# Kernel tuning notes

Hardware: AMD Instinct MI355X
Metric: run time of the kernel (lower is better)

Reference implementation:

```python
import jax, jax.numpy as jnp
import numpy as np

B, T, D, H = 2, 2048, 512, 8
HD = D // H  # head_dim = 64


def setup_inputs() -> dict:
    key = jax.random.key(0)
    k1, k2, k3, k4 = jax.random.split(key, 4)
    scale = 1.0 / np.sqrt(D)
    x = jax.random.normal(k1, (B, T, D), dtype=jnp.float32)
    periods = jax.random.randint(k2, (B, H), 0, 64, dtype=jnp.int32)
    w_qkv = jax.random.normal(k3, (3 * D, D), dtype=jnp.float32) * scale
    b_qkv = jnp.zeros((3 * D,), dtype=jnp.float32)
    w_out = jax.random.normal(k4, (D, D), dtype=jnp.float32) * scale
    b_out = jnp.zeros((D,), dtype=jnp.float32)
    return {"x": x, "periods": periods, "w_qkv": w_qkv, "b_qkv": b_qkv,
            "w_out": w_out, "b_out": b_out}


def reference(x, periods, w_qkv, b_qkv, w_out, b_out):
    # qkv projection: (B,T,3D) -> (3,B,H,T,HD)
    qkv = x @ w_qkv.T + b_qkv
    qkv = qkv.reshape(B, T, 3, H, HD).transpose(2, 0, 3, 1, 4)
    q, k, v = qkv[0], qkv[1], qkv[2]

    # periodic-causal mask: valid iff j <= i and (i-j) % p == 0, p = max(period,1)
    i_idx = jnp.arange(T, dtype=jnp.int32)[:, None]   # (T,1)
    j_idx = jnp.arange(T, dtype=jnp.int32)[None, :]   # (1,T)
    diff = i_idx - j_idx                              # (T,T)
    p = jnp.maximum(periods, 1)[:, :, None, None]     # (B,H,1,1)
    valid = (diff >= 0) & ((diff % p) == 0)           # (B,H,T,T)

    scores = jnp.einsum('bhqd,bhkd->bhqk', q, k) / np.sqrt(HD)
    scores = jnp.where(valid, scores, jnp.finfo(scores.dtype).min)
    attn = jax.nn.softmax(scores, axis=-1)

    out = jnp.einsum('bhqk,bhkd->bhqd', attn, v)
    out = out.transpose(0, 2, 1, 3).reshape(B, T, D)
    return out @ w_out.T + b_out
```

## Files before the change

### kernel.cpp

```cpp
#include <hip/hip_runtime.h>
#include <math.h>

#define B_  2
#define T_  2048
#define D_  512
#define H_  8
#define HD_ 64
#define QKVS (3*D_)

typedef __bf16 bf16x8 __attribute__((ext_vector_type(8)));
typedef float  f32x4  __attribute__((ext_vector_type(4)));

__device__ inline unsigned short f2bf(float f) {
  unsigned int u = __float_as_uint(f);
  return (unsigned short)((u + 0x7FFFu + ((u >> 16) & 1u)) >> 16);
}
__device__ inline unsigned int pack2bf(float lo, float hi) {
  return (unsigned int)f2bf(lo) | ((unsigned int)f2bf(hi) << 16);
}

__global__ void cast_all(const float* __restrict__ x,
                         const float* __restrict__ wq,
                         const float* __restrict__ wo,
                         unsigned short* __restrict__ xb,
                         unsigned short* __restrict__ wqb,
                         unsigned short* __restrict__ wob) {
  const int n_x  = (B_ * T_ * D_) / 4;
  const int n_wq = (QKVS * D_) / 4;
  const int n_wo = (D_ * D_) / 4;
  int i = blockIdx.x * blockDim.x + threadIdx.x;
  const float* src; unsigned short* dst; int off;
  if (i < n_x)                { src = x;  dst = xb;  off = i; }
  else if (i < n_x + n_wq)    { src = wq; dst = wqb; off = i - n_x; }
  else if (i < n_x + n_wq + n_wo) { src = wo; dst = wob; off = i - n_x - n_wq; }
  else return;
  float4 v = ((const float4*)src)[off];
  ushort4 o;
  o.x = f2bf(v.x); o.y = f2bf(v.y); o.z = f2bf(v.z); o.w = f2bf(v.w);
  ((ushort4*)dst)[off] = o;
}

template<int BF16OUT>
__global__ __launch_bounds__(256)
void gemm_nt_mfma(const unsigned short* __restrict__ A,
                  const unsigned short* __restrict__ Bw,
                  const float* __restrict__ bias, void* __restrict__ Cv,
                  int M, int N, int K) {
  __shared__ short Asd[128 * 32];
  __shared__ short Bsd[64 * 32];

  const int tid = threadIdx.x;
  const int w   = tid >> 6;
  const int l   = tid & 63;
  const int wr  = w >> 1;
  const int wc  = w & 1;
  const int q   = l >> 4;
  const int ml  = l & 15;
  const int arow = l >> 2;
  const int kch  = (l & 3) * 8;

  const int rowbase = blockIdx.y * 128;
  const int colbase = blockIdx.x * 64;

  f32x4 acc[4][2] = {};

  for (int k0 = 0; k0 < K; k0 += 32) {
    __syncthreads();
    #pragma unroll
    for (int s = 0; s < 2; ++s) {
      const unsigned short* g =
          A + (size_t)(rowbase + s * 64 + w * 16 + arow) * K + k0 + kch;
      short* lp = &Asd[s * 2048 + w * 512];
      __builtin_amdgcn_global_load_lds(
          (const __attribute__((address_space(1))) void*)g,
          (__attribute__((address_space(3))) void*)lp, 16, 0, 0);
    }
    {
      const unsigned short* g =
          Bw + (size_t)(colbase + w * 16 + arow) * K + k0 + kch;
      short* lp = &Bsd[w * 512];
      __builtin_amdgcn_global_load_lds(
          (const __attribute__((address_space(1))) void*)g,
          (__attribute__((address_space(3))) void*)lp, 16, 0, 0);
    }
    __syncthreads();

    bf16x8 af[4], bfr[2];
    #pragma unroll
    for (int mi = 0; mi < 4; ++mi)
      af[mi] = *(const bf16x8*)&Asd[(wr * 64 + mi * 16 + ml) * 32 + q * 8];
    #pragma unroll
    for (int ni = 0; ni < 2; ++ni)
      bfr[ni] = *(const bf16x8*)&Bsd[(wc * 32 + ni * 16 + ml) * 32 + q * 8];
    #pragma unroll
    for (int mi = 0; mi < 4; ++mi)
      #pragma unroll
      for (int ni = 0; ni < 2; ++ni)
        acc[mi][ni] = __builtin_amdgcn_mfma_f32_16x16x32_bf16(
            af[mi], bfr[ni], acc[mi][ni], 0, 0, 0);
  }

  #pragma unroll
  for (int mi = 0; mi < 4; ++mi) {
    #pragma unroll
    for (int ni = 0; ni < 2; ++ni) {
      const int col = colbase + wc * 32 + ni * 16 + ml;
      const float bv = bias[col];
      #pragma unroll
      for (int r = 0; r < 4; ++r) {
        const int row = rowbase + wr * 64 + mi * 16 + q * 4 + r;
        const float val = acc[mi][ni][r] + bv;
        if (BF16OUT)
          ((unsigned short*)Cv)[(size_t)row * N + col] = f2bf(val);
        else
          ((float*)Cv)[(size_t)row * N + col] = val;
      }
    }
  }
}

template<int BF16OUT>
__global__ __launch_bounds__(256)
void gemm_nt_mfma128(const unsigned short* __restrict__ A,
                     const unsigned short* __restrict__ Bw,
                     const float* __restrict__ bias, void* __restrict__ Cv,
                     int M, int N, int K) {
  __shared__ short Asd[128 * 32];
  __shared__ short Bsd[128 * 32];

  const int tid = threadIdx.x;
  const int w   = tid >> 6;
  const int l   = tid & 63;
  const int wr  = w >> 1;
  const int wc  = w & 1;
  const int q   = l >> 4;
  const int ml  = l & 15;
  const int arow = l >> 2;
  const int kch  = (l & 3) * 8;

  const int rowbase = blockIdx.y * 128;
  const int colbase = blockIdx.x * 128;

  f32x4 acc[4][4] = {};

  for (int k0 = 0; k0 < K; k0 += 32) {
    __syncthreads();
    #pragma unroll
    for (int s = 0; s < 2; ++s) {
      const unsigned short* ga =
          A + (size_t)(rowbase + s * 64 + w * 16 + arow) * K + k0 + kch;
      __builtin_amdgcn_global_load_lds(
          (const __attribute__((address_space(1))) void*)ga,
          (__attribute__((address_space(3))) void*)&Asd[s * 2048 + w * 512],
          16, 0, 0);
      const unsigned short* gb =
          Bw + (size_t)(colbase + s * 64 + w * 16 + arow) * K + k0 + kch;
      __builtin_amdgcn_global_load_lds(
          (const __attribute__((address_space(1))) void*)gb,
          (__attribute__((address_space(3))) void*)&Bsd[s * 2048 + w * 512],
          16, 0, 0);
    }
    __syncthreads();

    bf16x8 af[4], bfr[4];
    #pragma unroll
    for (int mi = 0; mi < 4; ++mi)
      af[mi] = *(const bf16x8*)&Asd[(wr * 64 + mi * 16 + ml) * 32 + q * 8];
    #pragma unroll
    for (int ni = 0; ni < 4; ++ni)
      bfr[ni] = *(const bf16x8*)&Bsd[(wc * 64 + ni * 16 + ml) * 32 + q * 8];
    #pragma unroll
    for (int mi = 0; mi < 4; ++mi)
      #pragma unroll
      for (int ni = 0; ni < 4; ++ni)
        acc[mi][ni] = __builtin_amdgcn_mfma_f32_16x16x32_bf16(
            af[mi], bfr[ni], acc[mi][ni], 0, 0, 0);
  }

  #pragma unroll
  for (int mi = 0; mi < 4; ++mi) {
    #pragma unroll
    for (int ni = 0; ni < 4; ++ni) {
      const int col = colbase + wc * 64 + ni * 16 + ml;
      const float bv = bias[col];
      #pragma unroll
      for (int r = 0; r < 4; ++r) {
        const int row = rowbase + wr * 64 + mi * 16 + q * 4 + r;
        const float val = acc[mi][ni][r] + bv;
        if (BF16OUT)
          ((unsigned short*)Cv)[(size_t)row * N + col] = f2bf(val);
        else
          ((float*)Cv)[(size_t)row * N + col] = val;
      }
    }
  }
}

__global__ __launch_bounds__(256)
void attn_flash2(const unsigned short* __restrict__ qkv,
                 const int* __restrict__ periods,
                 unsigned short* __restrict__ ao) {
  const int bh = blockIdx.x, slot = blockIdx.y;
  int p = periods[bh]; if (p < 1) p = 1;
  const int g  = slot / p;
  const int r  = slot - g * p;
  const int L  = (T_ - 1 - r) / p + 1;
  const int q0 = g << 6;
  if (q0 >= L) return;
  const int b = bh >> 3, h = bh & 7;
  const int Lrem = L - q0;
  const int Nkb  = min(L, q0 + 64);

  const int tid  = threadIdx.x;
  const int w    = tid >> 6;
  const int lane = tid & 63;
  const int Q = lane >> 4, c = lane & 15;

  __shared__ __align__(16) unsigned short Qs[64 * 72];
  __shared__ __align__(16) unsigned short Ks[32 * 72];
  __shared__ __align__(16) unsigned short Vt[64 * 40];

  const size_t rowb = (size_t)b * T_ * QKVS + (size_t)h * HD_;

  {
    const int u = tid >> 2, ch4 = (tid & 3) * 16;
    const int t = q0 + min(u, Lrem - 1);
    const unsigned short* gq = qkv + rowb + (size_t)(r + t * p) * QKVS + ch4;
    int4 v0 = ((const int4*)gq)[0];
    int4 v1 = ((const int4*)gq)[1];
    *(int4*)&Qs[u * 72 + ch4 + 0] = v0;
    *(int4*)&Qs[u * 72 + ch4 + 8] = v1;
  }
  __syncthreads();
  bf16x8 qf[2];
  qf[0] = *(const bf16x8*)&Qs[(w * 16 + c) * 72 + Q * 8];
  qf[1] = *(const bf16x8*)&Qs[(w * 16 + c) * 72 + Q * 8 + 32];

  const int qb      = w * 16;
  const int nqw     = min(16, Lrem - qb);
  const int qglob   = q0 + qb + c;
  const int mylastk = q0 + qb + 15;

  float m_run = -3.0e38f, l_run = 0.f;
  f32x4 o[4] = {};
  const size_t kb = rowb + D_;
  const size_t vb = rowb + 2 * D_;

  const int krow = tid >> 3, koff = (tid & 7) * 8;
  const int vkey = tid & 31, vd0 = (tid >> 5) * 8;

  for (int k0 = 0; k0 < Nkb; k0 += 32) {
    {
      const int tk = min(k0 + krow, Nkb - 1);
      const int tv = min(k0 + vkey, Nkb - 1);
      int4 kv = *(const int4*)(qkv + kb + (size_t)(r + tk * p) * QKVS + koff);
      int4 vv = *(const int4*)(qkv + vb + (size_t)(r + tv * p) * QKVS + vd0);
      unsigned short vh[8];
      *(int4*)vh = vv;
      __syncthreads();
      *(int4*)&Ks[krow * 72 + koff] = kv;
      #pragma unroll
      for (int j = 0; j < 8; ++j)
        Vt[(vd0 + j) * 40 + vkey] = vh[j];
      __syncthreads();
    }

    if (nqw > 0 && k0 <= mylastk) {
      f32x4 s[2];
      #pragma unroll
      for (int mt = 0; mt < 2; ++mt) {
        bf16x8 a0 = *(const bf16x8*)&Ks[(mt * 16 + c) * 72 + Q * 8];
        bf16x8 a1 = *(const bf16x8*)&Ks[(mt * 16 + c) * 72 + Q * 8 + 32];
        f32x4 acc = {};
        acc = __builtin_amdgcn_mfma_f32_16x16x32_bf16(a0, qf[0], acc, 0, 0, 0);
        acc = __builtin_amdgcn_mfma_f32_16x16x32_bf16(a1, qf[1], acc, 0, 0, 0);
        s[mt] = acc;
      }

      float pvv[8];
      float tmax = -3.0e38f;
      #pragma unroll
      for (int mt = 0; mt < 2; ++mt)
        #pragma unroll
        for (int rg = 0; rg < 4; ++rg) {
          const int kk = k0 + mt * 16 + Q * 4 + rg;
          float v = s[mt][rg] * 0.125f;
          v = (kk <= qglob) ? v : -3.0e38f;
          pvv[mt * 4 + rg] = v;
          tmax = fmaxf(tmax, v);
        }
      tmax = fmaxf(tmax, __shfl_xor(tmax, 16));
      tmax = fmaxf(tmax, __shfl_xor(tmax, 32));
      const float m_new = fmaxf(m_run, tmax);
      const float alpha = __expf(m_run - m_new);
      float tsum = 0.f;
      #pragma unroll
      for (int i = 0; i < 8; ++i) { pvv[i] = __expf(pvv[i] - m_new); tsum += pvv[i]; }
      tsum += __shfl_xor(tsum, 16);
      tsum += __shfl_xor(tsum, 32);
      l_run = l_run * alpha + tsum;
      m_run = m_new;

      unsigned int pk0[2], pk1[2];
      pk0[0] = pack2bf(pvv[0], pvv[1]); pk0[1] = pack2bf(pvv[2], pvv[3]);
      pk1[0] = pack2bf(pvv[4], pvv[5]); pk1[1] = pack2bf(pvv[6], pvv[7]);
      int dw[4];
      const int sq2 = (Q & 1) << 1;
      #pragma unroll
      for (int d = 0; d < 4; ++d) {
        const int src = ((sq2 + (d >> 1)) << 4) + c;
        const int v0 = __shfl((int)pk0[d & 1], src);
        const int v1 = __shfl((int)pk1[d & 1], src);
        dw[d] = (Q >= 2) ? v1 : v0;
      }
      int4 bi = make_int4(dw[0], dw[1], dw[2], dw[3]);
      bf16x8 pb = *(bf16x8*)&bi;

      #pragma unroll
      for (int ch = 0; ch < 4; ++ch) {
        bf16x8 af = *(const bf16x8*)&Vt[(ch * 16 + c) * 40 + Q * 8];
        f32x4 oo = o[ch];
        #pragma unroll
        for (int t2 = 0; t2 < 4; ++t2) oo[t2] *= alpha;
        o[ch] = __builtin_amdgcn_mfma_f32_16x16x32_bf16(af, pb, oo, 0, 0, 0);
      }
    }
  }

  if (nqw > 0 && c < nqw) {
    const float invl = 1.f / l_run;
    const int tok = r + (q0 + qb + c) * p;
    unsigned int* dst =
        (unsigned int*)(ao + (size_t)(b * T_ + tok) * D_ + h * HD_);
    #pragma unroll
    for (int ch = 0; ch < 4; ++ch)
      #pragma unroll
      for (int rp = 0; rp < 2; ++rp) {
        const int dhalf = ch * 16 + Q * 4 + rp * 2;
        dst[dhalf >> 1] =
            pack2bf(o[ch][rp * 2] * invl, o[ch][rp * 2 + 1] * invl);
      }
  }
}

extern "C" void kernel_launch(void* const* d_in, const int* in_sizes, int n_in,
                              void* d_out, int out_size, void* d_ws, size_t ws_size,
                              hipStream_t stream) {
  const float* x      = (const float*)d_in[0];
  const int*   period = (const int*)  d_in[1];
  const float* w_qkv  = (const float*)d_in[2];
  const float* b_qkv  = (const float*)d_in[3];
  const float* w_out  = (const float*)d_in[4];
  const float* b_out  = (const float*)d_in[5];
  float* out = (float*)d_out;

  const int M = B_ * T_;

  char* ws = (char*)d_ws;
  unsigned short* xb   = (unsigned short*)(ws);
  unsigned short* wqb  = (unsigned short*)(ws + (size_t)M * D_ * 2);
  unsigned short* wob  = (unsigned short*)(ws + (size_t)M * D_ * 2
                                              + (size_t)QKVS * D_ * 2);
  unsigned short* qkvb = (unsigned short*)(ws + (size_t)M * D_ * 2
                                              + (size_t)QKVS * D_ * 2
                                              + (size_t)D_ * D_ * 2);
  unsigned short* aob  = xb;

  {
    const int n4 = (M * D_ + QKVS * D_ + D_ * D_) / 4;
    cast_all<<<dim3((n4 + 255) / 256), dim3(256), 0, stream>>>(
        x, w_qkv, w_out, xb, wqb, wob);
  }

  gemm_nt_mfma128<1><<<dim3(QKVS / 128, M / 128), dim3(256), 0, stream>>>(
      xb, wqb, b_qkv, qkvb, M, QKVS, D_);

  attn_flash2<<<dim3(16, 63), dim3(256), 0, stream>>>(qkvb, period, aob);

  gemm_nt_mfma<0><<<dim3(D_ / 64, M / 128), dim3(256), 0, stream>>>(
      aob, wob, b_out, out, M, D_, D_);
}
```

Before: 116.6 us.

## Scatter QKV into period-grouped contiguous planes and use single-wave attention tiles

```diff
diff --git a/kernel.cpp b/kernel.cpp
--- a/kernel.cpp
+++ b/kernel.cpp
@@ -30,8 +30,8 @@
   const int n_wo = (D_ * D_) / 4;
   int i = blockIdx.x * blockDim.x + threadIdx.x;
   const float* src; unsigned short* dst; int off;
-  if (i < n_x)                { src = x;  dst = xb;  off = i; }
-  else if (i < n_x + n_wq)    { src = wq; dst = wqb; off = i - n_x; }
+  if (i < n_x)                    { src = x;  dst = xb;  off = i; }
+  else if (i < n_x + n_wq)        { src = wq; dst = wqb; off = i - n_x; }
   else if (i < n_x + n_wq + n_wo) { src = wo; dst = wob; off = i - n_x - n_wq; }
   else return;
   float4 v = ((const float4*)src)[off];
@@ -40,91 +40,15 @@
   ((ushort4*)dst)[off] = o;
 }
 
-template<int BF16OUT>
 __global__ __launch_bounds__(256)
-void gemm_nt_mfma(const unsigned short* __restrict__ A,
-                  const unsigned short* __restrict__ Bw,
-                  const float* __restrict__ bias, void* __restrict__ Cv,
-                  int M, int N, int K) {
-  __shared__ short Asd[128 * 32];
-  __shared__ short Bsd[64 * 32];
-
-  const int tid = threadIdx.x;
-  const int w   = tid >> 6;
-  const int l   = tid & 63;
-  const int wr  = w >> 1;
-  const int wc  = w & 1;
-  const int q   = l >> 4;
-  const int ml  = l & 15;
-  const int arow = l >> 2;
-  const int kch  = (l & 3) * 8;
-
-  const int rowbase = blockIdx.y * 128;
-  const int colbase = blockIdx.x * 64;
-
-  f32x4 acc[4][2] = {};
-
-  for (int k0 = 0; k0 < K; k0 += 32) {
-    __syncthreads();
-    #pragma unroll
-    for (int s = 0; s < 2; ++s) {
-      const unsigned short* g =
-          A + (size_t)(rowbase + s * 64 + w * 16 + arow) * K + k0 + kch;
-      short* lp = &Asd[s * 2048 + w * 512];
-      __builtin_amdgcn_global_load_lds(
-          (const __attribute__((address_space(1))) void*)g,
-          (__attribute__((address_space(3))) void*)lp, 16, 0, 0);
-    }
-    {
-      const unsigned short* g =
-          Bw + (size_t)(colbase + w * 16 + arow) * K + k0 + kch;
-      short* lp = &Bsd[w * 512];
-      __builtin_amdgcn_global_load_lds(
-          (const __attribute__((address_space(1))) void*)g,
-          (__attribute__((address_space(3))) void*)lp, 16, 0, 0);
-    }
-    __syncthreads();
-
-    bf16x8 af[4], bfr[2];
-    #pragma unroll
-    for (int mi = 0; mi < 4; ++mi)
-      af[mi] = *(const bf16x8*)&Asd[(wr * 64 + mi * 16 + ml) * 32 + q * 8];
-    #pragma unroll
-    for (int ni = 0; ni < 2; ++ni)
-      bfr[ni] = *(const bf16x8*)&Bsd[(wc * 32 + ni * 16 + ml) * 32 + q * 8];
-    #pragma unroll
-    for (int mi = 0; mi < 4; ++mi)
-      #pragma unroll
-      for (int ni = 0; ni < 2; ++ni)
-        acc[mi][ni] = __builtin_amdgcn_mfma_f32_16x16x32_bf16(
-            af[mi], bfr[ni], acc[mi][ni], 0, 0, 0);
-  }
-
-  #pragma unroll
-  for (int mi = 0; mi < 4; ++mi) {
-    #pragma unroll
-    for (int ni = 0; ni < 2; ++ni) {
-      const int col = colbase + wc * 32 + ni * 16 + ml;
-      const float bv = bias[col];
-      #pragma unroll
-      for (int r = 0; r < 4; ++r) {
-        const int row = rowbase + wr * 64 + mi * 16 + q * 4 + r;
-        const float val = acc[mi][ni][r] + bv;
-        if (BF16OUT)
-          ((unsigned short*)Cv)[(size_t)row * N + col] = f2bf(val);
-        else
-          ((float*)Cv)[(size_t)row * N + col] = val;
-      }
-    }
-  }
-}
-
-template<int BF16OUT>
-__global__ __launch_bounds__(256)
-void gemm_nt_mfma128(const unsigned short* __restrict__ A,
-                     const unsigned short* __restrict__ Bw,
-                     const float* __restrict__ bias, void* __restrict__ Cv,
-                     int M, int N, int K) {
+void gemm_qkv(const unsigned short* __restrict__ A,
+              const unsigned short* __restrict__ Bw,
+              const float* __restrict__ bias,
+              const int* __restrict__ periods,
+              unsigned short* __restrict__ Qr,
+              unsigned short* __restrict__ Kr,
+              unsigned short* __restrict__ Vr,
+              int M, int N, int K) {
   __shared__ short Asd[128 * 32];
   __shared__ short Bsd[128 * 32];
 
@@ -177,135 +101,161 @@
             af[mi], bfr[ni], acc[mi][ni], 0, 0, 0);
   }
 
+  const int colb = colbase + wc * 64;
+  const int sec  = colb >> 9;
+  const int h    = (colb >> 6) & 7;
+  const int bidx = rowbase >> 11;
+  unsigned short* plane =
+      (sec == 0 ? Qr : (sec == 1 ? Kr : Vr)) +
+      (size_t)(bidx * 8 + h) * (T_ * HD_);
+  unsigned int pp = (unsigned int)periods[bidx * 8 + h];
+  if ((int)pp < 1) pp = 1;
+  const unsigned int qd = 2048u / pp;
+  const unsigned int md = 2048u - qd * pp;
+
   #pragma unroll
   for (int mi = 0; mi < 4; ++mi) {
     #pragma unroll
-    for (int ni = 0; ni < 4; ++ni) {
-      const int col = colbase + wc * 64 + ni * 16 + ml;
-      const float bv = bias[col];
-      #pragma unroll
-      for (int r = 0; r < 4; ++r) {
-        const int row = rowbase + wr * 64 + mi * 16 + q * 4 + r;
-        const float val = acc[mi][ni][r] + bv;
-        if (BF16OUT)
-          ((unsigned short*)Cv)[(size_t)row * N + col] = f2bf(val);
-        else
-          ((float*)Cv)[(size_t)row * N + col] = val;
+    for (int r2 = 0; r2 < 4; ++r2) {
+      const unsigned int t =
+          (unsigned int)((rowbase + wr * 64 + mi * 16 + q * 4 + r2) & 2047);
+      const unsigned int ti = t / pp;
+      const unsigned int rr = t - ti * pp;
+      const unsigned int pos = rr * qd + (rr < md ? rr : md) + ti;
+      #pragma unroll
+      for (int ni = 0; ni < 4; ++ni) {
+        const int col = colb + ni * 16 + ml;
+        plane[(size_t)pos * HD_ + ni * 16 + ml] =
+            f2bf(acc[mi][ni][r2] + bias[col]);
       }
     }
   }
 }
 
 __global__ __launch_bounds__(256)
-void attn_flash2(const unsigned short* __restrict__ qkv,
+void transpose_v(const unsigned short* __restrict__ Vr,
+                 unsigned short* __restrict__ VTr) {
+  const int bh = blockIdx.x, chunk = blockIdx.y;
+  const int pos0 = chunk * 128;
+  __shared__ unsigned short Ls[128 * 72];
+  const int tid = threadIdx.x;
+  {
+    const int row = tid >> 1, off = (tid & 1) * 32;
+    const unsigned short* src = Vr + ((size_t)bh * T_ + pos0 + row) * HD_ + off;
+    int4 v0 = ((const int4*)src)[0];
+    int4 v1 = ((const int4*)src)[1];
+    int4 v2 = ((const int4*)src)[2];
+    int4 v3 = ((const int4*)src)[3];
+    *(int4*)&Ls[row * 72 + off + 0]  = v0;
+    *(int4*)&Ls[row * 72 + off + 8]  = v1;
+    *(int4*)&Ls[row * 72 + off + 16] = v2;
+    *(int4*)&Ls[row * 72 + off + 24] = v3;
+  }
+  __syncthreads();
+  {
+    const int d = tid >> 2, po = (tid & 3) * 32;
+    unsigned int wv[16];
+    #pragma unroll
+    for (int i = 0; i < 16; ++i) {
+      unsigned short lo = Ls[(po + 2 * i) * 72 + d];
+      unsigned short hi = Ls[(po + 2 * i + 1) * 72 + d];
+      wv[i] = (unsigned int)lo | ((unsigned int)hi << 16);
+    }
+    unsigned short* dst = VTr + ((size_t)bh * HD_ + d) * T_ + pos0 + po;
+    ((int4*)dst)[0] = make_int4(wv[0],  wv[1],  wv[2],  wv[3]);
+    ((int4*)dst)[1] = make_int4(wv[4],  wv[5],  wv[6],  wv[7]);
+    ((int4*)dst)[2] = make_int4(wv[8],  wv[9],  wv[10], wv[11]);
+    ((int4*)dst)[3] = make_int4(wv[12], wv[13], wv[14], wv[15]);
+  }
+}
+
+__global__ __launch_bounds__(64)
+void attn_flash3(const unsigned short* __restrict__ Qr,
+                 const unsigned short* __restrict__ Kr,
+                 const unsigned short* __restrict__ VTr,
                  const int* __restrict__ periods,
                  unsigned short* __restrict__ ao) {
   const int bh = blockIdx.x, slot = blockIdx.y;
   int p = periods[bh]; if (p < 1) p = 1;
-  const int g  = slot / p;
-  const int r  = slot - g * p;
-  const int L  = (T_ - 1 - r) / p + 1;
-  const int q0 = g << 6;
+  const int g = slot / p;
+  const int r = slot - g * p;
+  const unsigned int qd = 2048u / (unsigned int)p;
+  const unsigned int md = 2048u - qd * (unsigned int)p;
+  const int L = (int)qd + (r < (int)md ? 1 : 0);
+  const int q0 = g << 4;
   if (q0 >= L) return;
-  const int b = bh >> 3, h = bh & 7;
-  const int Lrem = L - q0;
-  const int Nkb  = min(L, q0 + 64);
-
-  const int tid  = threadIdx.x;
-  const int w    = tid >> 6;
-  const int lane = tid & 63;
+  const int off = r * (int)qd + min(r, (int)md);
+  const int nq = min(16, L - q0);
+  const int Nk = min(L, q0 + 16);
+
+  const int lane = threadIdx.x;
   const int Q = lane >> 4, c = lane & 15;
 
-  __shared__ __align__(16) unsigned short Qs[64 * 72];
-  __shared__ __align__(16) unsigned short Ks[32 * 72];
-  __shared__ __align__(16) unsigned short Vt[64 * 40];
-
-  const size_t rowb = (size_t)b * T_ * QKVS + (size_t)h * HD_;
-
-  {
-    const int u = tid >> 2, ch4 = (tid & 3) * 16;
-    const int t = q0 + min(u, Lrem - 1);
-    const unsigned short* gq = qkv + rowb + (size_t)(r + t * p) * QKVS + ch4;
-    int4 v0 = ((const int4*)gq)[0];
-    int4 v1 = ((const int4*)gq)[1];
-    *(int4*)&Qs[u * 72 + ch4 + 0] = v0;
-    *(int4*)&Qs[u * 72 + ch4 + 8] = v1;
-  }
-  __syncthreads();
-  bf16x8 qf[2];
-  qf[0] = *(const bf16x8*)&Qs[(w * 16 + c) * 72 + Q * 8];
-  qf[1] = *(const bf16x8*)&Qs[(w * 16 + c) * 72 + Q * 8 + 32];
-
-  const int qb      = w * 16;
-  const int nqw     = min(16, Lrem - qb);
-  const int qglob   = q0 + qb + c;
-  const int mylastk = q0 + qb + 15;
-
+  const unsigned short* Qp = Qr  + (size_t)bh * (T_ * HD_);
+  const unsigned short* Kp = Kr  + (size_t)bh * (T_ * HD_);
+  const unsigned short* Vp = VTr + (size_t)bh * (T_ * HD_);
+
+  const int qpos = off + q0 + min(c, nq - 1);
+  bf16x8 qf0 = *(const bf16x8*)(Qp + (size_t)qpos * HD_ + Q * 8);
+  bf16x8 qf1 = *(const bf16x8*)(Qp + (size_t)qpos * HD_ + 32 + Q * 8);
+
+  const int qglob = q0 + c;
   float m_run = -3.0e38f, l_run = 0.f;
   f32x4 o[4] = {};
-  const size_t kb = rowb + D_;
-  const size_t vb = rowb + 2 * D_;
-
-  const int krow = tid >> 3, koff = (tid & 7) * 8;
-  const int vkey = tid & 31, vd0 = (tid >> 5) * 8;
-
-  for (int k0 = 0; k0 < Nkb; k0 += 32) {
-    {
-      const int tk = min(k0 + krow, Nkb - 1);
-      const int tv = min(k0 + vkey, Nkb - 1);
-      int4 kv = *(const int4*)(qkv + kb + (size_t)(r + tk * p) * QKVS + koff);
-      int4 vv = *(const int4*)(qkv + vb + (size_t)(r + tv * p) * QKVS + vd0);
-      unsigned short vh[8];
-      *(int4*)vh = vv;
-      __syncthreads();
-      *(int4*)&Ks[krow * 72 + koff] = kv;
-      #pragma unroll
-      for (int j = 0; j < 8; ++j)
-        Vt[(vd0 + j) * 40 + vkey] = vh[j];
-      __syncthreads();
-    }
-
-    if (nqw > 0 && k0 <= mylastk) {
-      f32x4 s[2];
-      #pragma unroll
-      for (int mt = 0; mt < 2; ++mt) {
-        bf16x8 a0 = *(const bf16x8*)&Ks[(mt * 16 + c) * 72 + Q * 8];
-        bf16x8 a1 = *(const bf16x8*)&Ks[(mt * 16 + c) * 72 + Q * 8 + 32];
-        f32x4 acc = {};
-        acc = __builtin_amdgcn_mfma_f32_16x16x32_bf16(a0, qf[0], acc, 0, 0, 0);
-        acc = __builtin_amdgcn_mfma_f32_16x16x32_bf16(a1, qf[1], acc, 0, 0, 0);
-        s[mt] = acc;
-      }
-
-      float pvv[8];
-      float tmax = -3.0e38f;
-      #pragma unroll
-      for (int mt = 0; mt < 2; ++mt)
+
+  for (int k0 = 0; k0 < Nk; k0 += 64) {
+    const int nt = min(4, (Nk - k0 + 15) >> 4);
+
+    float pvv[16];
+    float tmax = -3.0e38f;
+    #pragma unroll
+    for (int mt = 0; mt < 4; ++mt) {
+      if (mt < nt) {
+        const int kpos = off + min(k0 + mt * 16 + c, Nk - 1);
+        bf16x8 a0 = *(const bf16x8*)(Kp + (size_t)kpos * HD_ + Q * 8);
+        bf16x8 a1 = *(const bf16x8*)(Kp + (size_t)kpos * HD_ + 32 + Q * 8);
+        f32x4 s = {};
+        s = __builtin_amdgcn_mfma_f32_16x16x32_bf16(a0, qf0, s, 0, 0, 0);
+        s = __builtin_amdgcn_mfma_f32_16x16x32_bf16(a1, qf1, s, 0, 0, 0);
         #pragma unroll
         for (int rg = 0; rg < 4; ++rg) {
           const int kk = k0 + mt * 16 + Q * 4 + rg;
-          float v = s[mt][rg] * 0.125f;
+          float v = s[rg] * 0.125f;
           v = (kk <= qglob) ? v : -3.0e38f;
           pvv[mt * 4 + rg] = v;
           tmax = fmaxf(tmax, v);
         }
-      tmax = fmaxf(tmax, __shfl_xor(tmax, 16));
-      tmax = fmaxf(tmax, __shfl_xor(tmax, 32));
-      const float m_new = fmaxf(m_run, tmax);
-      const float alpha = __expf(m_run - m_new);
-      float tsum = 0.f;
-      #pragma unroll
-      for (int i = 0; i < 8; ++i) { pvv[i] = __expf(pvv[i] - m_new); tsum += pvv[i]; }
-      tsum += __shfl_xor(tsum, 16);
-      tsum += __shfl_xor(tsum, 32);
-      l_run = l_run * alpha + tsum;
-      m_run = m_new;
-
+      } else {
+        #pragma unroll
+        for (int rg = 0; rg < 4; ++rg) pvv[mt * 4 + rg] = -3.0e38f;
+      }
+    }
+
+    tmax = fmaxf(tmax, __shfl_xor(tmax, 16));
+    tmax = fmaxf(tmax, __shfl_xor(tmax, 32));
+    const float m_new = fmaxf(m_run, tmax);
+    const float alpha = __expf(m_run - m_new);
+    float tsum = 0.f;
+    #pragma unroll
+    for (int i = 0; i < 16; ++i) {
+      pvv[i] = __expf(pvv[i] - m_new);
+      tsum += pvv[i];
+    }
+    tsum += __shfl_xor(tsum, 16);
+    tsum += __shfl_xor(tsum, 32);
+    l_run = l_run * alpha + tsum;
+    m_run = m_new;
+
+    bf16x8 pb[2];
+    const int sq2 = (Q & 1) << 1;
+    #pragma unroll
+    for (int kc = 0; kc < 2; ++kc) {
       unsigned int pk0[2], pk1[2];
-      pk0[0] = pack2bf(pvv[0], pvv[1]); pk0[1] = pack2bf(pvv[2], pvv[3]);
-      pk1[0] = pack2bf(pvv[4], pvv[5]); pk1[1] = pack2bf(pvv[6], pvv[7]);
+      pk0[0] = pack2bf(pvv[kc * 8 + 0], pvv[kc * 8 + 1]);
+      pk0[1] = pack2bf(pvv[kc * 8 + 2], pvv[kc * 8 + 3]);
+      pk1[0] = pack2bf(pvv[kc * 8 + 4], pvv[kc * 8 + 5]);
+      pk1[1] = pack2bf(pvv[kc * 8 + 6], pvv[kc * 8 + 7]);
       int dw[4];
-      const int sq2 = (Q & 1) << 1;
       #pragma unroll
       for (int d = 0; d < 4; ++d) {
         const int src = ((sq2 + (d >> 1)) << 4) + c;
@@ -314,22 +264,32 @@
         dw[d] = (Q >= 2) ? v1 : v0;
       }
       int4 bi = make_int4(dw[0], dw[1], dw[2], dw[3]);
-      bf16x8 pb = *(bf16x8*)&bi;
-
-      #pragma unroll
-      for (int ch = 0; ch < 4; ++ch) {
-        bf16x8 af = *(const bf16x8*)&Vt[(ch * 16 + c) * 40 + Q * 8];
-        f32x4 oo = o[ch];
+      pb[kc] = *(bf16x8*)&bi;
+    }
+
+    #pragma unroll
+    for (int ch = 0; ch < 4; ++ch) {
+      #pragma unroll
+      for (int t2 = 0; t2 < 4; ++t2) o[ch][t2] *= alpha;
+    }
+    #pragma unroll
+    for (int kc = 0; kc < 2; ++kc) {
+      if (k0 + kc * 32 < Nk) {
         #pragma unroll
-        for (int t2 = 0; t2 < 4; ++t2) oo[t2] *= alpha;
-        o[ch] = __builtin_amdgcn_mfma_f32_16x16x32_bf16(af, pb, oo, 0, 0, 0);
-      }
-    }
-  }
-
-  if (nqw > 0 && c < nqw) {
+        for (int ch = 0; ch < 4; ++ch) {
+          bf16x8 af = *(const bf16x8*)(
+              Vp + (size_t)(ch * 16 + c) * T_ + off + k0 + kc * 32 + Q * 8);
+          o[ch] = __builtin_amdgcn_mfma_f32_16x16x32_bf16(af, pb[kc], o[ch],
+                                                          0, 0, 0);
+        }
+      }
+    }
+  }
+
+  if (c < nq) {
     const float invl = 1.f / l_run;
-    const int tok = r + (q0 + qb + c) * p;
+    const int b = bh >> 3, h = bh & 7;
+    const int tok = r + (q0 + c) * p;
     unsigned int* dst =
         (unsigned int*)(ao + (size_t)(b * T_ + tok) * D_ + h * HD_);
     #pragma unroll
@@ -340,6 +300,79 @@
         dst[dhalf >> 1] =
             pack2bf(o[ch][rp * 2] * invl, o[ch][rp * 2 + 1] * invl);
       }
+  }
+}
+
+__global__ __launch_bounds__(256)
+void gemm_out(const unsigned short* __restrict__ A,
+              const unsigned short* __restrict__ Bw,
+              const float* __restrict__ bias, float* __restrict__ C,
+              int M, int N, int K) {
+  __shared__ short Asd[128 * 32];
+  __shared__ short Bsd[64 * 32];
+
+  const int tid = threadIdx.x;
+  const int w   = tid >> 6;
+  const int l   = tid & 63;
+  const int wr  = w >> 1;
+  const int wc  = w & 1;
+  const int q   = l >> 4;
+  const int ml  = l & 15;
+  const int arow = l >> 2;
+  const int kch  = (l & 3) * 8;
+
+  const int rowbase = blockIdx.y * 128;
+  const int colbase = blockIdx.x * 64;
+
+  f32x4 acc[4][2] = {};
+
+  for (int k0 = 0; k0 < K; k0 += 32) {
+    __syncthreads();
+    #pragma unroll
+    for (int s = 0; s < 2; ++s) {
+      const unsigned short* ga =
+          A + (size_t)(rowbase + s * 64 + w * 16 + arow) * K + k0 + kch;
+      __builtin_amdgcn_global_load_lds(
+          (const __attribute__((address_space(1))) void*)ga,
+          (__attribute__((address_space(3))) void*)&Asd[s * 2048 + w * 512],
+          16, 0, 0);
+    }
+    {
+      const unsigned short* gb =
+          Bw + (size_t)(colbase + w * 16 + arow) * K + k0 + kch;
+      __builtin_amdgcn_global_load_lds(
+          (const __attribute__((address_space(1))) void*)gb,
+          (__attribute__((address_space(3))) void*)&Bsd[w * 512], 16, 0, 0);
+    }
+    __syncthreads();
+
+    bf16x8 af[4], bfr[2];
+    #pragma unroll
+    for (int mi = 0; mi < 4; ++mi)
+      af[mi] = *(const bf16x8*)&Asd[(wr * 64 + mi * 16 + ml) * 32 + q * 8];
+    #pragma unroll
+    for (int ni = 0; ni < 2; ++ni)
+      bfr[ni] = *(const bf16x8*)&Bsd[(wc * 32 + ni * 16 + ml) * 32 + q * 8];
+    #pragma unroll
+    for (int mi = 0; mi < 4; ++mi)
+      #pragma unroll
+      for (int ni = 0; ni < 2; ++ni)
+        acc[mi][ni] = __builtin_amdgcn_mfma_f32_16x16x32_bf16(
+            af[mi], bfr[ni], acc[mi][ni], 0, 0, 0);
+  }
+
+  #pragma unroll
+  for (int mi = 0; mi < 4; ++mi) {
+    #pragma unroll
+    for (int ni = 0; ni < 2; ++ni) {
+      const int col = colbase + wc * 32 + ni * 16 + ml;
+      const float bv = bias[col];
+      #pragma unroll
+      for (int r = 0; r < 4; ++r) {
+        const int row = rowbase + wr * 64 + mi * 16 + q * 4 + r;
+        C[(size_t)row * N + col] = acc[mi][ni][r] + bv;
+      }
+    }
   }
 }
 
@@ -357,14 +390,18 @@
   const int M = B_ * T_;
 
   char* ws = (char*)d_ws;
-  unsigned short* xb   = (unsigned short*)(ws);
-  unsigned short* wqb  = (unsigned short*)(ws + (size_t)M * D_ * 2);
-  unsigned short* wob  = (unsigned short*)(ws + (size_t)M * D_ * 2
-                                              + (size_t)QKVS * D_ * 2);
-  unsigned short* qkvb = (unsigned short*)(ws + (size_t)M * D_ * 2
-                                              + (size_t)QKVS * D_ * 2
-                                              + (size_t)D_ * D_ * 2);
-  unsigned short* aob  = xb;
+  unsigned short* xb  = (unsigned short*)(ws);
+  unsigned short* wqb = (unsigned short*)(ws + (size_t)M * D_ * 2);
+  unsigned short* wob = (unsigned short*)(ws + (size_t)M * D_ * 2
+                                             + (size_t)QKVS * D_ * 2);
+  char* base6 = ws + (size_t)M * D_ * 2 + (size_t)QKVS * D_ * 2
+                   + (size_t)D_ * D_ * 2;
+  const size_t plane_bytes = (size_t)16 * T_ * HD_ * 2;
+  unsigned short* Qr  = (unsigned short*)(base6);
+  unsigned short* Kr  = (unsigned short*)(base6 + plane_bytes);
+  unsigned short* Vr  = (unsigned short*)(base6 + 2 * plane_bytes);
+  unsigned short* VTr = (unsigned short*)(base6 + 3 * plane_bytes);
+  unsigned short* aob = xb;
 
   {
     const int n4 = (M * D_ + QKVS * D_ + D_ * D_) / 4;
@@ -372,11 +409,14 @@
         x, w_qkv, w_out, xb, wqb, wob);
   }
 
-  gemm_nt_mfma128<1><<<dim3(QKVS / 128, M / 128), dim3(256), 0, stream>>>(
-      xb, wqb, b_qkv, qkvb, M, QKVS, D_);
-
-  attn_flash2<<<dim3(16, 63), dim3(256), 0, stream>>>(qkvb, period, aob);
-
-  gemm_nt_mfma<0><<<dim3(D_ / 64, M / 128), dim3(256), 0, stream>>>(
+  gemm_qkv<<<dim3(QKVS / 128, M / 128), dim3(256), 0, stream>>>(
+      xb, wqb, b_qkv, period, Qr, Kr, Vr, M, QKVS, D_);
+
+  transpose_v<<<dim3(16, T_ / 128), dim3(256), 0, stream>>>(Vr, VTr);
+
+  attn_flash3<<<dim3(16, 192), dim3(64), 0, stream>>>(
+      Qr, Kr, VTr, period, aob);
+
+  gemm_out<<<dim3(D_ / 64, M / 128), dim3(256), 0, stream>>>(
       aob, wob, b_out, out, M, D_, D_);
 }
```

New measurement: 136.3 us. 16.8% more time.

## Replace LDS-staged GEMMs with direct-global-load register double-buffered MFMA GEMM

Applied to the files above, without the earlier changes.

```diff
diff --git a/kernel.cpp b/kernel.cpp
--- a/kernel.cpp
+++ b/kernel.cpp
@@ -30,8 +30,8 @@
   const int n_wo = (D_ * D_) / 4;
   int i = blockIdx.x * blockDim.x + threadIdx.x;
   const float* src; unsigned short* dst; int off;
-  if (i < n_x)                { src = x;  dst = xb;  off = i; }
-  else if (i < n_x + n_wq)    { src = wq; dst = wqb; off = i - n_x; }
+  if (i < n_x)                    { src = x;  dst = xb;  off = i; }
+  else if (i < n_x + n_wq)        { src = wq; dst = wqb; off = i - n_x; }
   else if (i < n_x + n_wq + n_wo) { src = wo; dst = wob; off = i - n_x - n_wq; }
   else return;
   float4 v = ((const float4*)src)[off];
@@ -40,152 +40,64 @@
   ((ushort4*)dst)[off] = o;
 }
 
-template<int BF16OUT>
-__global__ __launch_bounds__(256)
-void gemm_nt_mfma(const unsigned short* __restrict__ A,
-                  const unsigned short* __restrict__ Bw,
-                  const float* __restrict__ bias, void* __restrict__ Cv,
-                  int M, int N, int K) {
-  __shared__ short Asd[128 * 32];
-  __shared__ short Bsd[64 * 32];
-
+template<int BF16OUT, int KSTEPS>
+__global__ __launch_bounds__(256, 3)
+void gemm_nt_direct(const unsigned short* __restrict__ A,
+                    const unsigned short* __restrict__ Bw,
+                    const float* __restrict__ bias, void* __restrict__ Cv,
+                    int M, int N, int K) {
   const int tid = threadIdx.x;
-  const int w   = tid >> 6;
-  const int l   = tid & 63;
-  const int wr  = w >> 1;
-  const int wc  = w & 1;
-  const int q   = l >> 4;
-  const int ml  = l & 15;
-  const int arow = l >> 2;
-  const int kch  = (l & 3) * 8;
-
-  const int rowbase = blockIdx.y * 128;
-  const int colbase = blockIdx.x * 64;
-
-  f32x4 acc[4][2] = {};
-
-  for (int k0 = 0; k0 < K; k0 += 32) {
-    __syncthreads();
+  const int w  = tid >> 6, l = tid & 63;
+  const int wr = w >> 1,  wc = w & 1;
+  const int Q  = l >> 4,  c  = l & 15;
+  const int rowbase = blockIdx.y * 64  + wr * 32;
+  const int colbase = blockIdx.x * 128 + wc * 64;
+
+  int aoff[2], boff[4];
+  #pragma unroll
+  for (int mi = 0; mi < 2; ++mi)
+    aoff[mi] = (rowbase + mi * 16 + c) * K + Q * 8;
+  #pragma unroll
+  for (int ni = 0; ni < 4; ++ni)
+    boff[ni] = (colbase + ni * 16 + c) * K + Q * 8;
+
+  f32x4 acc[2][4] = {};
+  bf16x8 af[2][2], bf[2][4];
+
+  #pragma unroll
+  for (int mi = 0; mi < 2; ++mi) af[0][mi] = *(const bf16x8*)(A  + aoff[mi]);
+  #pragma unroll
+  for (int ni = 0; ni < 4; ++ni) bf[0][ni] = *(const bf16x8*)(Bw + boff[ni]);
+
+  #pragma unroll
+  for (int s = 0; s < KSTEPS; ++s) {
+    const int cur = s & 1, nxt = cur ^ 1;
+    if (s < KSTEPS - 1) {
+      const int k1 = (s + 1) * 32;
+      #pragma unroll
+      for (int mi = 0; mi < 2; ++mi)
+        af[nxt][mi] = *(const bf16x8*)(A + aoff[mi] + k1);
+      #pragma unroll
+      for (int ni = 0; ni < 4; ++ni)
+        bf[nxt][ni] = *(const bf16x8*)(Bw + boff[ni] + k1);
+    }
     #pragma unroll
-    for (int s = 0; s < 2; ++s) {
-      const unsigned short* g =
-          A + (size_t)(rowbase + s * 64 + w * 16 + arow) * K + k0 + kch;
-      short* lp = &Asd[s * 2048 + w * 512];
-      __builtin_amdgcn_global_load_lds(
-          (const __attribute__((address_space(1))) void*)g,
-          (__attribute__((address_space(3))) void*)lp, 16, 0, 0);
-    }
-    {
-      const unsigned short* g =
-          Bw + (size_t)(colbase + w * 16 + arow) * K + k0 + kch;
-      short* lp = &Bsd[w * 512];
-      __builtin_amdgcn_global_load_lds(
-          (const __attribute__((address_space(1))) void*)g,
-          (__attribute__((address_space(3))) void*)lp, 16, 0, 0);
-    }
-    __syncthreads();
-
-    bf16x8 af[4], bfr[2];
-    #pragma unroll
-    for (int mi = 0; mi < 4; ++mi)
-      af[mi] = *(const bf16x8*)&Asd[(wr * 64 + mi * 16 + ml) * 32 + q * 8];
-    #pragma unroll
-    for (int ni = 0; ni < 2; ++ni)
-      bfr[ni] = *(const bf16x8*)&Bsd[(wc * 32 + ni * 16 + ml) * 32 + q * 8];
-    #pragma unroll
-    for (int mi = 0; mi < 4; ++mi)
-      #pragma unroll
-      for (int ni = 0; ni < 2; ++ni)
-        acc[mi][ni] = __builtin_amdgcn_mfma_f32_16x16x32_bf16(
-            af[mi], bfr[ni], acc[mi][ni], 0, 0, 0);
-  }
-
-  #pragma unroll
-  for (int mi = 0; mi < 4; ++mi) {
-    #pragma unroll
-    for (int ni = 0; ni < 2; ++ni) {
-      const int col = colbase + wc * 32 + ni * 16 + ml;
-      const float bv = bias[col];
-      #pragma unroll
-      for (int r = 0; r < 4; ++r) {
-        const int row = rowbase + wr * 64 + mi * 16 + q * 4 + r;
-        const float val = acc[mi][ni][r] + bv;
-        if (BF16OUT)
-          ((unsigned short*)Cv)[(size_t)row * N + col] = f2bf(val);
-        else
-          ((float*)Cv)[(size_t)row * N + col] = val;
-      }
-    }
-  }
-}
-
-template<int BF16OUT>
-__global__ __launch_bounds__(256)
-void gemm_nt_mfma128(const unsigned short* __restrict__ A,
-                     const unsigned short* __restrict__ Bw,
-                     const float* __restrict__ bias, void* __restrict__ Cv,
-                     int M, int N, int K) {
-  __shared__ short Asd[128 * 32];
-  __shared__ short Bsd[128 * 32];
-
-  const int tid = threadIdx.x;
-  const int w   = tid >> 6;
-  const int l   = tid & 63;
-  const int wr  = w >> 1;
-  const int wc  = w & 1;
-  const int q   = l >> 4;
-  const int ml  = l & 15;
-  const int arow = l >> 2;
-  const int kch  = (l & 3) * 8;
-
-  const int rowbase = blockIdx.y * 128;
-  const int colbase = blockIdx.x * 128;
-
-  f32x4 acc[4][4] = {};
-
-  for (int k0 = 0; k0 < K; k0 += 32) {
-    __syncthreads();
-    #pragma unroll
-    for (int s = 0; s < 2; ++s) {
-      const unsigned short* ga =
-          A + (size_t)(rowbase + s * 64 + w * 16 + arow) * K + k0 + kch;
-      __builtin_amdgcn_global_load_lds(
-          (const __attribute__((address_space(1))) void*)ga,
-          (__attribute__((address_space(3))) void*)&Asd[s * 2048 + w * 512],
-          16, 0, 0);
-      const unsigned short* gb =
-          Bw + (size_t)(colbase + s * 64 + w * 16 + arow) * K + k0 + kch;
-      __builtin_amdgcn_global_load_lds(
-          (const __attribute__((address_space(1))) void*)gb,
-          (__attribute__((address_space(3))) void*)&Bsd[s * 2048 + w * 512],
-          16, 0, 0);
-    }
-    __syncthreads();
-
-    bf16x8 af[4], bfr[4];
-    #pragma unroll
-    for (int mi = 0; mi < 4; ++mi)
-      af[mi] = *(const bf16x8*)&Asd[(wr * 64 + mi * 16 + ml) * 32 + q * 8];
-    #pragma unroll
-    for (int ni = 0; ni < 4; ++ni)
-      bfr[ni] = *(const bf16x8*)&Bsd[(wc * 64 + ni * 16 + ml) * 32 + q * 8];
-    #pragma unroll
-    for (int mi = 0; mi < 4; ++mi)
+    for (int mi = 0; mi < 2; ++mi)
       #pragma unroll
       for (int ni = 0; ni < 4; ++ni)
         acc[mi][ni] = __builtin_amdgcn_mfma_f32_16x16x32_bf16(
-            af[mi], bfr[ni], acc[mi][ni], 0, 0, 0);
-  }
-
-  #pragma unroll
-  for (int mi = 0; mi < 4; ++mi) {
+            af[cur][mi], bf[cur][ni], acc[mi][ni], 0, 0, 0);
+  }
+
+  #pragma unroll
+  for (int mi = 0; mi < 2; ++mi) {
     #pragma unroll
     for (int ni = 0; ni < 4; ++ni) {
-      const int col = colbase + wc * 64 + ni * 16 + ml;
+      const int col = colbase + ni * 16 + c;
       const float bv = bias[col];
       #pragma unroll
       for (int r = 0; r < 4; ++r) {
-        const int row = rowbase + wr * 64 + mi * 16 + q * 4 + r;
+        const int row = rowbase + mi * 16 + Q * 4 + r;
         const float val = acc[mi][ni][r] + bv;
         if (BF16OUT)
           ((unsigned short*)Cv)[(size_t)row * N + col] = f2bf(val);
@@ -372,11 +284,11 @@
         x, w_qkv, w_out, xb, wqb, wob);
   }
 
-  gemm_nt_mfma128<1><<<dim3(QKVS / 128, M / 128), dim3(256), 0, stream>>>(
+  gemm_nt_direct<1, 16><<<dim3(QKVS / 128, M / 64), dim3(256), 0, stream>>>(
       xb, wqb, b_qkv, qkvb, M, QKVS, D_);
 
   attn_flash2<<<dim3(16, 63), dim3(256), 0, stream>>>(qkvb, period, aob);
 
-  gemm_nt_mfma<0><<<dim3(D_ / 64, M / 128), dim3(256), 0, stream>>>(
+  gemm_nt_direct<0, 16><<<dim3(D_ / 128, M / 64), dim3(256), 0, stream>>>(
       aob, wob, b_out, out, M, D_, D_);
 }
```

Result: slower. 135.6 us (+16.2%).

## Prefetch next K/V tile into registers and reverse attention block order

Applied to the files above, without the earlier changes.

```diff
diff --git a/kernel.cpp b/kernel.cpp
--- a/kernel.cpp
+++ b/kernel.cpp
@@ -30,8 +30,8 @@
   const int n_wo = (D_ * D_) / 4;
   int i = blockIdx.x * blockDim.x + threadIdx.x;
   const float* src; unsigned short* dst; int off;
-  if (i < n_x)                { src = x;  dst = xb;  off = i; }
-  else if (i < n_x + n_wq)    { src = wq; dst = wqb; off = i - n_x; }
+  if (i < n_x)                    { src = x;  dst = xb;  off = i; }
+  else if (i < n_x + n_wq)        { src = wq; dst = wqb; off = i - n_x; }
   else if (i < n_x + n_wq + n_wo) { src = wo; dst = wob; off = i - n_x - n_wq; }
   else return;
   float4 v = ((const float4*)src)[off];
@@ -70,18 +70,17 @@
     for (int s = 0; s < 2; ++s) {
       const unsigned short* g =
           A + (size_t)(rowbase + s * 64 + w * 16 + arow) * K + k0 + kch;
-      short* lp = &Asd[s * 2048 + w * 512];
       __builtin_amdgcn_global_load_lds(
           (const __attribute__((address_space(1))) void*)g,
-          (__attribute__((address_space(3))) void*)lp, 16, 0, 0);
+          (__attribute__((address_space(3))) void*)&Asd[s * 2048 + w * 512],
+          16, 0, 0);
     }
     {
       const unsigned short* g =
           Bw + (size_t)(colbase + w * 16 + arow) * K + k0 + kch;
-      short* lp = &Bsd[w * 512];
       __builtin_amdgcn_global_load_lds(
           (const __attribute__((address_space(1))) void*)g,
-          (__attribute__((address_space(3))) void*)lp, 16, 0, 0);
+          (__attribute__((address_space(3))) void*)&Bsd[w * 512], 16, 0, 0);
     }
     __syncthreads();
 
@@ -200,7 +199,7 @@
 void attn_flash2(const unsigned short* __restrict__ qkv,
                  const int* __restrict__ periods,
                  unsigned short* __restrict__ ao) {
-  const int bh = blockIdx.x, slot = blockIdx.y;
+  const int bh = blockIdx.x, slot = 62 - blockIdx.y;
   int p = periods[bh]; if (p < 1) p = 1;
   const int g  = slot / p;
   const int r  = slot - g * p;
@@ -249,20 +248,31 @@
   const int krow = tid >> 3, koff = (tid & 7) * 8;
   const int vkey = tid & 31, vd0 = (tid >> 5) * 8;
 
+  int4 kvp, vvp;
+  {
+    const int tk = min(krow, Nkb - 1);
+    const int tv = min(vkey, Nkb - 1);
+    kvp = *(const int4*)(qkv + kb + (size_t)(r + tk * p) * QKVS + koff);
+    vvp = *(const int4*)(qkv + vb + (size_t)(r + tv * p) * QKVS + vd0);
+  }
+
   for (int k0 = 0; k0 < Nkb; k0 += 32) {
+    __syncthreads();
     {
-      const int tk = min(k0 + krow, Nkb - 1);
-      const int tv = min(k0 + vkey, Nkb - 1);
-      int4 kv = *(const int4*)(qkv + kb + (size_t)(r + tk * p) * QKVS + koff);
-      int4 vv = *(const int4*)(qkv + vb + (size_t)(r + tv * p) * QKVS + vd0);
       unsigned short vh[8];
-      *(int4*)vh = vv;
-      __syncthreads();
-      *(int4*)&Ks[krow * 72 + koff] = kv;
+      *(int4*)vh = vvp;
+      *(int4*)&Ks[krow * 72 + koff] = kvp;
       #pragma unroll
       for (int j = 0; j < 8; ++j)
         Vt[(vd0 + j) * 40 + vkey] = vh[j];
-      __syncthreads();
+    }
+    __syncthreads();
+
+    if (k0 + 32 < Nkb) {
+      const int tk = min(k0 + 32 + krow, Nkb - 1);
+      const int tv = min(k0 + 32 + vkey, Nkb - 1);
+      kvp = *(const int4*)(qkv + kb + (size_t)(r + tk * p) * QKVS + koff);
+      vvp = *(const int4*)(qkv + vb + (size_t)(r + tv * p) * QKVS + vd0);
     }
 
     if (nqw > 0 && k0 <= mylastk) {
```

After: 113.4 us. -2.8%, faster.
